# Kernel optimization log

Measured on AMD Instinct MI355X. Metric: run time of the kernel, lower is better.

The kernel has to match this reference:

```python
import jax, jax.numpy as jnp
import numpy as np

H = 24        # attn.heads (Flux)
ENC = 512     # encoder (text) token count, hard-coded in the source via emb[:512]
EPS = 1e-6    # RMSNorm eps


def _rms(x, w):
    # RMSNorm over head_dim (Flux norm_q / norm_k)
    return x * jax.lax.rsqrt(jnp.mean(x * x, axis=-1, keepdims=True) + EPS) * w


def _rope(x, cos, sin):
    # diffusers apply_rotary_emb, use_real=True, unbind_dim=-1
    xr = x.reshape(x.shape[:-1] + (-1, 2))
    rot = jnp.stack([-xr[..., 1], xr[..., 0]], axis=-1).reshape(x.shape)
    return x * cos + rot * sin


def setup_inputs() -> dict:
    key = jax.random.key(0)
    ks = jax.random.split(key, 26)
    B, F, D = 2, 1024, 3072
    hd = D // H
    S = ENC + F
    lin = lambda k: 0.02 * jax.random.normal(k, (D, D), jnp.float32)
    bias = lambda k: 0.02 * jax.random.normal(k, (D,), jnp.float32)
    nw = lambda k: 1.0 + 0.02 * jax.random.normal(k, (hd,), jnp.float32)
    return {
        'hidden_states': jax.random.normal(ks[0], (B, F, D), jnp.float32),
        'encoder_hidden_states': jax.random.normal(ks[1], (B, ENC, D), jnp.float32),
        'rot_cos': jax.random.uniform(ks[2], (S, hd), jnp.float32, minval=-1.0, maxval=1.0),
        'rot_sin': jax.random.uniform(ks[3], (S, hd), jnp.float32, minval=-1.0, maxval=1.0),
        'wq': lin(ks[4]), 'bq': bias(ks[5]),
        'wk': lin(ks[6]), 'bk': bias(ks[7]),
        'wv': lin(ks[8]), 'bv': bias(ks[9]),
        'waq': lin(ks[10]), 'baq': bias(ks[11]),
        'wak': lin(ks[12]), 'bak': bias(ks[13]),
        'wav': lin(ks[14]), 'bav': bias(ks[15]),
        'wo': lin(ks[16]), 'bo': bias(ks[17]),
        'wao': lin(ks[18]), 'bao': bias(ks[19]),
        'nq': nw(ks[20]), 'nk': nw(ks[21]),
        'naq': nw(ks[22]), 'nak': nw(ks[23]),
    }


def reference(hidden_states, encoder_hidden_states, rot_cos, rot_sin,
              wq, bq, wk, bk, wv, bv, waq, baq, wak, bak, wav, bav,
              wo, bo, wao, bao, nq, nk, naq, nak):
    B, F, D = hidden_states.shape
    hd = D // H

    def proj(x, w, b):
        y = x @ w.T + b
        return y.reshape(x.shape[0], -1, H, hd).transpose(0, 2, 1, 3)  # [B,H,S,hd]

    q = _rms(proj(hidden_states, wq, bq), nq)   # [B,H,F,hd]
    k = _rms(proj(hidden_states, wk, bk), nk)
    v = proj(hidden_states, wv, bv)

    # cross-batch mixing: 'b h f d -> 1 h (b f) d' then repeat over batch
    k = jnp.broadcast_to(k.transpose(1, 0, 2, 3).reshape(1, H, B * F, hd), (B, H, B * F, hd))
    v = jnp.broadcast_to(v.transpose(1, 0, 2, 3).reshape(1, H, B * F, hd), (B, H, B * F, hd))

    # key rotary: encoder part once, image part repeated num_components times
    cos_k = jnp.concatenate([rot_cos[:ENC]] + [rot_cos[ENC:]] * B, axis=0)
    sin_k = jnp.concatenate([rot_sin[:ENC]] + [rot_sin[ENC:]] * B, axis=0)

    eq = _rms(proj(encoder_hidden_states, waq, baq), naq)  # [B,H,ENC,hd]
    ek = _rms(proj(encoder_hidden_states, wak, bak), nak)
    ev = proj(encoder_hidden_states, wav, bav)

    q = jnp.concatenate([eq, q], axis=2)  # [B,H,ENC+F,hd]
    k = jnp.concatenate([ek, k], axis=2)  # [B,H,ENC+B*F,hd]
    v = jnp.concatenate([ev, v], axis=2)

    q = _rope(q, rot_cos, rot_sin)
    k = _rope(k, cos_k, sin_k)

    scale = hd ** -0.5
    attn = jax.nn.softmax(jnp.einsum('bhqd,bhkd->bhqk', q, k) * scale, axis=-1)
    out = jnp.einsum('bhqk,bhkd->bhqd', attn, v)
    out = out.transpose(0, 2, 1, 3).reshape(B, -1, D)  # [B,ENC+F,D]

    enc_out = out[:, :ENC] @ wao.T + bao
    hs_out = out[:, ENC:] @ wo.T + bo
    return (hs_out, enc_out)
```

## Files before the change

kernel.cpp:

```cpp
#include <hip/hip_runtime.h>

typedef __attribute__((ext_vector_type(8))) short bf16x8;
typedef __attribute__((ext_vector_type(8))) unsigned short u16x8;
typedef __attribute__((ext_vector_type(4))) unsigned short u16x4;
typedef __attribute__((ext_vector_type(4))) float f32x4;
typedef __attribute__((ext_vector_type(2))) unsigned uint2v;

#define DEV static __device__ __forceinline__

DEV unsigned short f2bf(float f){
  unsigned u = __float_as_uint(f);
  u += 0x7fff + ((u>>16)&1);
  return (unsigned short)(u>>16);
}
DEV float bf2f(unsigned short b){ return __uint_as_float(((unsigned)b)<<16); }
DEV unsigned cvtpk(float lo, float hi){
  unsigned r;
  asm("v_cvt_pk_bf16_f32 %0, %1, %2" : "=v"(r) : "v"(lo), "v"(hi));
  return r;
}

DEV void gll16(const void* g, void* l){
  __builtin_amdgcn_global_load_lds((__attribute__((address_space(1))) unsigned*)(void*)g,
                                   (__attribute__((address_space(3))) unsigned*)l, 16, 0, 0);
}

__global__ void k_cast(const float* __restrict__ x, unsigned short* __restrict__ y, int n4){
  int i = blockIdx.x*256 + threadIdx.x;
  if (i >= n4) return;
  f32x4 v = ((const f32x4*)x)[i];
  u16x4 o = { f2bf(v.x), f2bf(v.y), f2bf(v.z), f2bf(v.w) };
  ((u16x4*)y)[i] = o;
}

__global__ void k_castX2(const float* __restrict__ s0, const float* __restrict__ s1,
                         unsigned short* __restrict__ y){
  unsigned i = blockIdx.x*256 + threadIdx.x;
  const float* s = (i < 1572864u) ? s0 : s1;
  unsigned off = (i < 1572864u) ? i : i - 1572864u;
  f32x4 v = ((const f32x4*)s)[off];
  u16x4 o = { f2bf(v.x), f2bf(v.y), f2bf(v.z), f2bf(v.w) };
  ((u16x4*)y)[i] = o;
}

__global__ void k_castAll(const float* __restrict__ s0, const float* __restrict__ s1,
                          const float* __restrict__ s2, const float* __restrict__ s3,
                          const float* __restrict__ s4, const float* __restrict__ s5,
                          const float* __restrict__ s6, const float* __restrict__ s7,
                          const float* __restrict__ xh, const float* __restrict__ xe,
                          unsigned short* __restrict__ Wb, unsigned short* __restrict__ Xc){
  unsigned i = blockIdx.x*256 + threadIdx.x;
  const float* s; unsigned off; unsigned short* dst; unsigned di;
  if (i < 18874368u){
    unsigned seg = i / 2359296u;
    off = i - seg*2359296u;
    s = seg==0?s0: seg==1?s1: seg==2?s2: seg==3?s3:
        seg==4?s4: seg==5?s5: seg==6?s6: s7;
    dst = Wb; di = i;
  } else {
    unsigned j = i - 18874368u;
    s = (j < 1572864u) ? xh : xe;
    off = (j < 1572864u) ? j : j - 1572864u;
    dst = Xc; di = j;
  }
  f32x4 v = ((const f32x4*)s)[off];
  u16x4 o = { f2bf(v.x), f2bf(v.y), f2bf(v.z), f2bf(v.w) };
  ((u16x4*)dst)[di] = o;
}

__global__ void k_castW2(const float* __restrict__ s0, const float* __restrict__ s1,
                         unsigned short* __restrict__ y){
  unsigned i = blockIdx.x*256 + threadIdx.x;
  unsigned seg = i / 2359296u;
  unsigned off = i - seg*2359296u;
  const float* s = seg==0?s0:s1;
  f32x4 v = ((const f32x4*)s)[off];
  u16x4 o = { f2bf(v.x), f2bf(v.y), f2bf(v.z), f2bf(v.w) };
  ((u16x4*)y)[i] = o;
}

__global__ __launch_bounds__(256) void k_gemmP(
    const unsigned short* __restrict__ X,
    const unsigned short* __restrict__ Wimg, const unsigned short* __restrict__ Wenc,
    const float* __restrict__ b0, const float* __restrict__ b1, const float* __restrict__ b2,
    const float* __restrict__ b3, const float* __restrict__ b4, const float* __restrict__ b5,
    const float* __restrict__ nq_, const float* __restrict__ nk_,
    const float* __restrict__ naq_, const float* __restrict__ nak_,
    const float* __restrict__ cs, const float* __restrict__ sn,
    unsigned short* __restrict__ Qd,
    unsigned short* __restrict__ Kdi, unsigned short* __restrict__ Kde,
    unsigned short* __restrict__ Vdi, unsigned short* __restrict__ Vde,
    int rows_img)
{
  const int K = 3072;
  __shared__ unsigned short SH[16384];
  unsigned short (*As)[4096] = (unsigned short(*)[4096])SH;
  unsigned short (*Bs)[4096] = (unsigned short(*)[4096])(SH + 8192);
  const int t = threadIdx.x, w = t>>6, l = t&63;
  const int li = l&15, g = l>>4;
  const int by = blockIdx.y, bx = blockIdx.x;
  const int sec = by>=48 ? 2 : (by>=24 ? 1 : 0);
  const int hd = by - sec*24;
  const int Cl = hd*128;
  const int R = bx*128;
  const bool img = (R < rows_img);
  const unsigned short* Wp = (img ? Wimg : Wenc) + (long)sec*9437184 + (long)Cl*K;
  const float* bias = img ? ((sec==0)?b0:(sec==1)?b1:b2)
                          : ((sec==0)?b3:(sec==1)?b4:b5);
  const int wr = w>>1, wc = w&1;
  f32x4 acc[4][4] = {};

  auto stage = [&](int buf, int kt){
    const int k0 = kt*32;
    #pragma unroll
    for (int c=0;c<2;c++){
      int row = c*64 + (t>>2);
      int scol = ((t&3)<<3) ^ ((row&3)<<3) ^ (((row>>3)&1)<<4);
      gll16(X + (long)(R+row)*K + k0 + scol, &As[buf][c*2048 + w*512]);
      gll16(Wp + (long)row*K + k0 + scol, &Bs[buf][c*2048 + w*512]);
    }
  };

  stage(0,0);
  int buf = 0;
  for (int kt=0; kt<96; kt++){
    __syncthreads();
    if (kt+1 < 96) stage(buf^1, kt+1);
    bf16x8 a[4], b[4];
    #pragma unroll
    for (int m=0;m<4;m++){
      int ar = wr*64 + m*16 + li;
      int ac = (g<<3) ^ ((ar&3)<<3) ^ (((ar>>3)&1)<<4);
      a[m] = *(const bf16x8*)&As[buf][ar*32 + ac];
      int br = wc*64 + m*16 + li;
      int bc2 = (g<<3) ^ ((br&3)<<3) ^ (((br>>3)&1)<<4);
      b[m] = *(const bf16x8*)&Bs[buf][br*32 + bc2];
    }
    #pragma unroll
    for (int m=0;m<4;m++)
      #pragma unroll
      for (int n=0;n<4;n++)
        acc[m][n] = __builtin_amdgcn_mfma_f32_16x16x32_bf16(a[m], b[n], acc[m][n], 0,0,0);
    buf ^= 1;
  }

  float bias_n[4];
  #pragma unroll
  for (int n=0;n<4;n++) bias_n[n] = bias[Cl + wc*64 + n*16 + li];

  if (sec == 2){
    unsigned short* SHT = SH;
    unsigned short* Vd = img ? Vdi : Vde;
    #pragma unroll
    for (int pass=0; pass<2; pass++){
      __syncthreads();
      if (wc == pass){
        #pragma unroll
        for (int m=0;m<4;m++){
          int tok_l = wr*64 + m*16 + (g<<2);
          #pragma unroll
          for (int n=0;n<4;n++){
            int col_loc = n*16 + li;
            u16x4 v4 = { f2bf(acc[m][n][0]+bias_n[n]), f2bf(acc[m][n][1]+bias_n[n]),
                         f2bf(acc[m][n][2]+bias_n[n]), f2bf(acc[m][n][3]+bias_n[n]) };
            *(u16x4*)&SHT[col_loc*136 + tok_l] = v4;
          }
        }
      }
      __syncthreads();
      int d_loc = t>>2, qtr = t&3;
      int d = pass*64 + d_loc;
      int tok0 = R + qtr*32;
      long base;
      if (img) base = ((long)hd*128 + d)*2048 + tok0;
      else { int t2 = tok0 - rows_img; int b_ = t2>>9, s_ = t2&511;
             base = ((long)(b_*24+hd)*128 + d)*512 + s_; }
      #pragma unroll
      for (int k2=0;k2<4;k2++)
        *(u16x8*)(Vd + base + k2*8) = *(const u16x8*)&SHT[d_loc*136 + qtr*32 + k2*8];
    }
    return;
  }

  float part[4][4];
  #pragma unroll
  for (int m=0;m<4;m++)
    #pragma unroll
    for (int r=0;r<4;r++){
      float s_ = 0.f;
      #pragma unroll
      for (int n=0;n<4;n++){ float v = acc[m][n][r] + bias_n[n]; s_ += v*v; }
      part[m][r] = s_;
    }
  #pragma unroll
  for (int m=0;m<4;m++)
    #pragma unroll
    for (int r=0;r<4;r++){
      part[m][r] += __shfl_xor(part[m][r], 1);
      part[m][r] += __shfl_xor(part[m][r], 2);
      part[m][r] += __shfl_xor(part[m][r], 4);
      part[m][r] += __shfl_xor(part[m][r], 8);
    }
  __syncthreads();
  float* rs = (float*)SH;
  if (li == 0){
    #pragma unroll
    for (int m=0;m<4;m++)
      #pragma unroll
      for (int r=0;r<4;r++)
        rs[(wc*2+wr)*64 + m*16 + g*4 + r] = part[m][r];
  }
  __syncthreads();
  float fac[4][4];
  #pragma unroll
  for (int m=0;m<4;m++)
    #pragma unroll
    for (int r=0;r<4;r++){
      int idx = m*16 + g*4 + r;
      float tot = rs[(0*2+wr)*64 + idx] + rs[(1*2+wr)*64 + idx];
      fac[m][r] = rsqrtf(tot*(1.0f/128.0f) + 1e-6f);
    }

  const float* nw = (sec==0) ? (img ? nq_ : naq_) : (img ? nk_ : nak_);
  const float qs = (sec==0) ? (float)(0.08838834764831845 * 1.4426950408889634) : 1.0f;
  float nw_n[4];
  #pragma unroll
  for (int n=0;n<4;n++) nw_n[n] = nw[wc*64 + n*16 + li];

  unsigned short* Kd = img ? Kdi : Kde;

  #pragma unroll
  for (int m=0;m<4;m++){
    #pragma unroll
    for (int r=0;r<4;r++){
      int row_l = wr*64 + m*16 + g*4 + r;
      int t_row = R + row_l;
      int b_, s_, p_;
      if (img){ b_ = t_row>>10; s_ = t_row&1023; p_ = 512+s_; }
      else { int t2 = t_row - rows_img; b_ = t2>>9; s_ = t2&511; p_ = s_; }
      long didx;
      if (sec==0) didx = (long)(b_*24+hd)*1536 + (img ? 512+s_ : s_);
      else        didx = img ? ((long)hd*2048 + t_row) : ((long)(b_*24+hd)*512 + s_);
      const float* crow = cs + (long)p_*128;
      const float* srow = sn + (long)p_*128;
      unsigned short* drow = ((sec==0)?Qd:Kd) + didx*128;
      #pragma unroll
      for (int n=0;n<4;n++){
        int cl = wc*64 + n*16 + li;
        float x = (acc[m][n][r] + bias_n[n]) * fac[m][r] * nw_n[n];
        float xo = __shfl_xor(x, 1);
        float o_ = x*crow[cl] + ((l&1) ? xo*srow[cl] : -xo*srow[cl]);
        drow[cl] = f2bf(o_*qs);
      }
    }
  }
}

__global__ __launch_bounds__(256) void k_gemmO(
    const unsigned short* __restrict__ X, const unsigned short* __restrict__ Wf,
    float* __restrict__ out, const float* __restrict__ bo, const float* __restrict__ bao)
{
  const int K = 3072;
  __shared__ unsigned short As[2][4096];
  __shared__ unsigned short Bs[2][4096];
  const int t = threadIdx.x, w = t>>6, l = t&63;
  unsigned wid = blockIdx.x + 24u*blockIdx.y;
  unsigned xc = wid & 7, ii = wid >> 3;
  unsigned xg = xc & 1, yg = xc >> 1;
  int bx = (int)(xg*12 + ii%12);
  int by = (int)(yg*6 + ii/12);
  const bool enc = bx >= 16;
  const unsigned short* Wp = Wf + (enc ? 9437184 : 0);
  const float* bias = enc ? bao : bo;
  const int R = bx*128, C = by*128;
  long xbase, obase;
  if (!enc){ xbase = (long)(R>>10)*1536 + 512 + (R&1023); obase = (long)R*3072; }
  else { int Rp = R-2048; xbase = (long)(Rp>>9)*1536 + (Rp&511); obase = 6291456 + (long)Rp*3072; }
  const int wr = w>>1, wc = w&1;
  f32x4 acc[4][4] = {};

  auto stage = [&](int buf, int kt){
    const int k0 = kt*32;
    #pragma unroll
    for (int c=0;c<2;c++){
      int row = c*64 + (t>>2);
      int scol = ((t&3)<<3) ^ ((row&3)<<3) ^ (((row>>3)&1)<<4);
      gll16(X + (xbase+row)*K + k0 + scol, &As[buf][c*2048 + w*512]);
      gll16(Wp + (long)(C+row)*K + k0 + scol, &Bs[buf][c*2048 + w*512]);
    }
  };

  stage(0,0);
  int buf = 0;
  for (int kt=0; kt<96; kt++){
    __syncthreads();
    if (kt+1 < 96) stage(buf^1, kt+1);
    bf16x8 a[4], b[4];
    #pragma unroll
    for (int m=0;m<4;m++){
      int ar = wr*64 + m*16 + (l&15);
      int ac = ((l>>4)<<3) ^ ((ar&3)<<3) ^ (((ar>>3)&1)<<4);
      a[m] = *(const bf16x8*)&As[buf][ar*32 + ac];
      int br = wc*64 + m*16 + (l&15);
      int bc2 = ((l>>4)<<3) ^ ((br&3)<<3) ^ (((br>>3)&1)<<4);
      b[m] = *(const bf16x8*)&Bs[buf][br*32 + bc2];
    }
    #pragma unroll
    for (int m=0;m<4;m++)
      #pragma unroll
      for (int n=0;n<4;n++)
        acc[m][n] = __builtin_amdgcn_mfma_f32_16x16x32_bf16(a[m], b[n], acc[m][n], 0,0,0);
    buf ^= 1;
  }

  #pragma unroll
  for (int m=0;m<4;m++){
    int rl = wr*64 + m*16 + ((l>>4)<<2);
    #pragma unroll
    for (int n=0;n<4;n++){
      int col = C + wc*64 + n*16 + (l&15);
      float bvv = bias[col];
      #pragma unroll
      for (int r=0;r<4;r++)
        out[obase + (long)(rl+r)*3072 + col] = acc[m][n][r] + bvv;
    }
  }
}

__global__ __launch_bounds__(256) void k_attn(
    const unsigned short* __restrict__ Q,
    const unsigned short* __restrict__ Ke, const unsigned short* __restrict__ Ki,
    const unsigned short* __restrict__ Ve, const unsigned short* __restrict__ Vi,
    unsigned short* __restrict__ AO)
{
  __shared__ unsigned short Ks[8192];
  __shared__ unsigned short Vs[8192];
  __shared__ unsigned short Ps[4][1408];
  const int t = threadIdx.x, w = t>>6, l = t&63;
  unsigned wid = blockIdx.x + 24u*blockIdx.y + 576u*blockIdx.z;
  unsigned xc = wid & 7, ii = wid >> 3;
  int h = (int)(xc*3 + ii/48);
  unsigned rem = ii % 48;
  int b = (int)(rem/24);
  int qx = (int)(rem%24);
  const int bh = b*24 + h;
  const int q0 = qx*64 + w*16;
  const int g = l>>4;

  auto stageK = [&](int jt){
    const unsigned short* ksrc = (jt < 8) ? Ke + ((long)bh*512 + jt*64)*128
                                          : Ki + ((long)h*2048 + (jt-8)*64)*128;
    #pragma unroll
    for (int c=0;c<4;c++){
      int row = c*16 + (t>>4);
      int col = ((t&15)<<3) ^ ((row&7)<<3);
      gll16(ksrc + row*128 + col, &Ks[c*2048 + w*512]);
    }
  };
  auto stageV = [&](int jt){
    const unsigned short* vsrc; long vstr;
    if (jt < 8){ vsrc = Ve + (long)bh*65536 + jt*64; vstr = 512; }
    else { vsrc = Vi + (long)h*262144 + (jt-8)*64; vstr = 2048; }
    #pragma unroll
    for (int c=0;c<4;c++){
      int row = c*32 + (t>>3);
      int col = ((t&7)<<3) ^ ((row&7)<<3);
      gll16(vsrc + (long)row*vstr + col, &Vs[c*2048 + w*512]);
    }
  };

  bf16x8 qf[4];
  {
    const unsigned short* qp = Q + ((long)bh*1536 + q0 + (l&15))*128 + (g<<3);
    #pragma unroll
    for (int kc=0;kc<4;kc++) qf[kc] = *(const bf16x8*)(qp + kc*32);
  }
  f32x4 o[8] = {};
  float mx = -1e30f;
  float ls = 0.f;

  stageK(0);
  for (int jt=0; jt<40; jt++){
    __syncthreads();
    stageV(jt);

    f32x4 sf[4];
    __builtin_amdgcn_s_setprio(1);
    #pragma unroll
    for (int ct=0;ct<4;ct++){
      f32x4 s = {};
      #pragma unroll
      for (int kc=0;kc<4;kc++){
        int krow = ct*16 + (l&15);
        int kcol = (kc*32 + (g<<3)) ^ ((krow&7)<<3);
        bf16x8 kb = *(const bf16x8*)&Ks[krow*128 + kcol];
        s = __builtin_amdgcn_mfma_f32_16x16x32_bf16(kb, qf[kc], s, 0,0,0);
      }
      sf[ct] = s;
    }
    __builtin_amdgcn_s_setprio(0);

    float pm = sf[0][0];
    #pragma unroll
    for (int ct=0;ct<4;ct++)
      #pragma unroll
      for (int r=0;r<4;r++) pm = fmaxf(pm, sf[ct][r]);
    if (!__all(pm <= mx + 8.0f)){
      float tmax = pm;
      tmax = fmaxf(tmax, __shfl_xor(tmax, 16));
      tmax = fmaxf(tmax, __shfl_xor(tmax, 32));
      float mn = fmaxf(mx, tmax);
      float al = exp2f(mx - mn);
      mx = mn;
      ls *= al;
      #pragma unroll
      for (int r=0;r<4;r++){
        float alo = __shfl(al, (l&48) | ((g<<2)+r));
        #pragma unroll
        for (int f=0;f<8;f++) o[f][r] *= alo;
      }
    }
    #pragma unroll
    for (int ct=0;ct<4;ct++){
      float p0 = exp2f(sf[ct][0]-mx), p1 = exp2f(sf[ct][1]-mx);
      float p2 = exp2f(sf[ct][2]-mx), p3 = exp2f(sf[ct][3]-mx);
      ls += (p0+p1)+(p2+p3);
      uint2v pk = { cvtpk(p0,p1), cvtpk(p2,p3) };
      *(uint2v*)&Ps[w][(l&15)*88 + ct*16 + (g<<2)] = pk;
    }
    __syncthreads();

    if (jt+1 < 40) stageK(jt+1);

    bf16x8 pa[2];
    #pragma unroll
    for (int kc=0;kc<2;kc++)
      pa[kc] = *(const bf16x8*)&Ps[w][(l&15)*88 + kc*32 + (g<<3)];
    __builtin_amdgcn_s_setprio(1);
    #pragma unroll
    for (int f=0;f<8;f++){
      #pragma unroll
      for (int kc=0;kc<2;kc++){
        int vrow = f*16 + (l&15);
        int vcol = (kc*32 + (g<<3)) ^ ((vrow&7)<<3);
        bf16x8 vb = *(const bf16x8*)&Vs[vrow*64 + vcol];
        o[f] = __builtin_amdgcn_mfma_f32_16x16x32_bf16(pa[kc], vb, o[f], 0,0,0);
      }
    }
    __builtin_amdgcn_s_setprio(0);
  }

  ls += __shfl_xor(ls, 16);
  ls += __shfl_xor(ls, 32);
  #pragma unroll
  for (int r=0;r<4;r++){
    float lso = __shfl(ls, (l&48) | ((g<<2)+r));
    float inv = 1.0f/lso;
    int qrow = q0 + (g<<2) + r;
    #pragma unroll
    for (int f=0;f<8;f++){
      AO[((long)b*1536 + qrow)*3072 + h*128 + f*16 + (l&15)] = f2bf(o[f][r]*inv);
    }
  }
}

extern "C" void kernel_launch(void* const* d_in, const int* in_sizes, int n_in,
                              void* d_out, int out_size, void* d_ws, size_t ws_size,
                              hipStream_t stream)
{
  const float* hs  = (const float*)d_in[0];
  const float* ehs = (const float*)d_in[1];
  const float* rc  = (const float*)d_in[2];
  const float* rs_ = (const float*)d_in[3];
  const float* wq = (const float*)d_in[4];  const float* bq = (const float*)d_in[5];
  const float* wk = (const float*)d_in[6];  const float* bk = (const float*)d_in[7];
  const float* wv = (const float*)d_in[8];  const float* bv = (const float*)d_in[9];
  const float* waq= (const float*)d_in[10]; const float* baq= (const float*)d_in[11];
  const float* wak= (const float*)d_in[12]; const float* bak= (const float*)d_in[13];
  const float* wav= (const float*)d_in[14]; const float* bav= (const float*)d_in[15];
  const float* wo = (const float*)d_in[16]; const float* bo = (const float*)d_in[17];
  const float* wao= (const float*)d_in[18]; const float* bao= (const float*)d_in[19];
  const float* nq = (const float*)d_in[20]; const float* nk = (const float*)d_in[21];
  const float* naq= (const float*)d_in[22]; const float* nak= (const float*)d_in[23];

  char* p = (char*)d_ws;
  auto alloc = [&](size_t bytes){ char* r = p; p += bytes; return r; };

  if (ws_size >= (size_t)226492416){
    unsigned short* Xh = (unsigned short*)alloc(12582912);
    unsigned short* Xe = (unsigned short*)alloc(6291456);
    unsigned short* Wb = (unsigned short*)alloc(150994944);
    unsigned short* Qb = (unsigned short*)alloc(18874368);
    unsigned short* Ke = (unsigned short*)alloc(6291456);
    unsigned short* Ki = (unsigned short*)alloc(12582912);
    unsigned short* Ve = (unsigned short*)alloc(6291456);
    unsigned short* Vi = (unsigned short*)alloc(12582912);
    unsigned short* AO = Xh;
    (void)Xe;

    k_castAll<<<82944,256,0,stream>>>(wq, wk, wv, waq, wak, wav, wo, wao, hs, ehs, Wb, Xh);

    k_gemmP<<<dim3(24,72),256,0,stream>>>(Xh, Wb, Wb + (long)3*9437184,
                                          bq, bk, bv, baq, bak, bav,
                                          nq, nk, naq, nak, rc, rs_,
                                          Qb, Ki, Ke, Vi, Ve, 2048);

    k_attn<<<dim3(24,24,2),256,0,stream>>>(Qb, Ke, Ki, Ve, Vi, AO);

    k_gemmO<<<dim3(24,24),256,0,stream>>>(AO, Wb + (long)6*9437184, (float*)d_out, bo, bao);
  } else {
    unsigned short* Xh = (unsigned short*)alloc(12582912);
    unsigned short* Xe = (unsigned short*)alloc(6291456);
    unsigned short* Wb = (unsigned short*)alloc(56623104);
    unsigned short* Qb = (unsigned short*)alloc(18874368);
    unsigned short* Ke = (unsigned short*)alloc(6291456);
    unsigned short* Ki = (unsigned short*)alloc(12582912);
    unsigned short* Ve = (unsigned short*)alloc(6291456);
    unsigned short* Vi = (unsigned short*)alloc(12582912);
    unsigned short* AO = Xh;

    k_castX2<<<9216,256,0,stream>>>(hs, ehs, Xh);

    k_cast<<<9216,256,0,stream>>>(wq, Wb, 2359296);
    k_cast<<<9216,256,0,stream>>>(wk, Wb + 9437184, 2359296);
    k_cast<<<9216,256,0,stream>>>(wv, Wb + 18874368, 2359296);
    k_gemmP<<<dim3(16,72),256,0,stream>>>(Xh, Wb, Wb,
                                          bq, bk, bv, bq, bk, bv,
                                          nq, nk, nq, nk, rc, rs_,
                                          Qb, Ki, Ke, Vi, Ve, 1<<28);

    k_cast<<<9216,256,0,stream>>>(waq, Wb, 2359296);
    k_cast<<<9216,256,0,stream>>>(wak, Wb + 9437184, 2359296);
    k_cast<<<9216,256,0,stream>>>(wav, Wb + 18874368, 2359296);
    k_gemmP<<<dim3(8,72),256,0,stream>>>(Xe, Wb, Wb,
                                         baq, bak, bav, baq, bak, bav,
                                         naq, nak, naq, nak, rc, rs_,
                                         Qb, Ki, Ke, Vi, Ve, 0);

    k_attn<<<dim3(24,24,2),256,0,stream>>>(Qb, Ke, Ki, Ve, Vi, AO);

    k_castW2<<<18432,256,0,stream>>>(wo, wao, Wb);
    k_gemmO<<<dim3(24,24),256,0,stream>>>(AO, Wb, (float*)d_out, bo, bao);
  }
}
```

Before: 654.9 us.

## Split QKV projection into 256x256-tile GEMM plus separate norm/rope/transposition passes

Replaces the fused projection GEMM (which applied RMSNorm, RoPE and layout writes in its epilogue) with a larger 256x256 tile, 512-thread GEMM that writes a plain bf16 Y buffer. Separate small kernels then apply RMSNorm+RoPE to Q/K, folding softmax scale times log2e into Q, and transpose V into the attention layout. The output-projection weight cast is moved to after attention so it reuses the weight buffer. This adds extra passes over the projection output and more launches in exchange for better tile reuse in the dominant GEMM, and it needs a larger workspace, otherwise the fallback path runs.

```diff
diff --git a/kernel.cpp b/kernel.cpp
--- a/kernel.cpp
+++ b/kernel.cpp
@@ -43,22 +43,20 @@
   ((u16x4*)y)[i] = o;
 }
 
-__global__ void k_castAll(const float* __restrict__ s0, const float* __restrict__ s1,
+__global__ void k_castA6X(const float* __restrict__ s0, const float* __restrict__ s1,
                           const float* __restrict__ s2, const float* __restrict__ s3,
                           const float* __restrict__ s4, const float* __restrict__ s5,
-                          const float* __restrict__ s6, const float* __restrict__ s7,
                           const float* __restrict__ xh, const float* __restrict__ xe,
                           unsigned short* __restrict__ Wb, unsigned short* __restrict__ Xc){
   unsigned i = blockIdx.x*256 + threadIdx.x;
   const float* s; unsigned off; unsigned short* dst; unsigned di;
-  if (i < 18874368u){
+  if (i < 14155776u){
     unsigned seg = i / 2359296u;
     off = i - seg*2359296u;
-    s = seg==0?s0: seg==1?s1: seg==2?s2: seg==3?s3:
-        seg==4?s4: seg==5?s5: seg==6?s6: s7;
+    s = seg==0?s0: seg==1?s1: seg==2?s2: seg==3?s3: seg==4?s4: s5;
     dst = Wb; di = i;
   } else {
-    unsigned j = i - 18874368u;
+    unsigned j = i - 14155776u;
     s = (j < 1572864u) ? xh : xe;
     off = (j < 1572864u) ? j : j - 1572864u;
     dst = Xc; di = j;
@@ -77,6 +75,160 @@
   f32x4 v = ((const f32x4*)s)[off];
   u16x4 o = { f2bf(v.x), f2bf(v.y), f2bf(v.z), f2bf(v.w) };
   ((u16x4*)y)[i] = o;
+}
+
+__global__ __launch_bounds__(512) void k_gemmP256(
+    const unsigned short* __restrict__ X,
+    const unsigned short* __restrict__ Wimg, const unsigned short* __restrict__ Wenc,
+    const float* __restrict__ b0, const float* __restrict__ b1, const float* __restrict__ b2,
+    const float* __restrict__ b3, const float* __restrict__ b4, const float* __restrict__ b5,
+    unsigned short* __restrict__ Y, int rows_img)
+{
+  __shared__ unsigned short LDS[2][32768];
+  const int t = threadIdx.x, w = t>>6, l = t&63;
+  const int li = l&15, g = l>>4;
+  const int wr = w>>2, wc = w&3;
+  const int bxr = blockIdx.x, by = blockIdx.y;
+  const int R = bxr*256;
+  const int sec = by/12;
+  const int Cn = (by%12)*256;
+  const bool img = (R < rows_img);
+  const unsigned short* Wbase = (img ? Wimg : Wenc) + (long)sec*9437184 + (long)Cn*3072;
+  const float* bias = img ? ((sec==0)?b0:(sec==1)?b1:b2)
+                          : ((sec==0)?b3:(sec==1)?b4:b5);
+
+  f32x4 acc[8][4] = {};
+
+  auto stageC = [&](int buf, int kt, int c){
+    int row = (c&3)*64 + (t>>3);
+    int sgrp = (t&7) ^ (row&7);
+    const unsigned short* src = (c<4)
+        ? X + (long)(R+row)*3072 + kt*64 + sgrp*8
+        : Wbase + (long)row*3072 + kt*64 + sgrp*8;
+    gll16(src, &LDS[buf][(c<4?0:16384) + (c&3)*4096 + t*8]);
+  };
+
+  #pragma unroll
+  for (int c=0;c<8;c++) stageC(0, 0, c);
+
+  for (int kt=0; kt<48; kt++){
+    __syncthreads();
+    const int buf = kt&1;
+    const unsigned short* Ab = &LDS[buf][0];
+    const unsigned short* Bb = &LDS[buf][16384];
+
+    bf16x8 Bf[4][2];
+    #pragma unroll
+    for (int fc=0;fc<4;fc++)
+      #pragma unroll
+      for (int kh=0;kh<2;kh++){
+        int brow = wc*64 + fc*16 + li;
+        int bgrp = ((kh<<2) + g) ^ (brow&7);
+        Bf[fc][kh] = *(const bf16x8*)&Bb[brow*64 + bgrp*8];
+      }
+    if (kt+1 < 48){
+      #pragma unroll
+      for (int c=0;c<4;c++) stageC(buf^1, kt+1, c);
+    }
+
+    #pragma unroll
+    for (int p=0;p<4;p++){
+      bf16x8 Af[2][2];
+      #pragma unroll
+      for (int f2=0;f2<2;f2++)
+        #pragma unroll
+        for (int kh=0;kh<2;kh++){
+          int arow = wr*128 + (2*p+f2)*16 + li;
+          int agrp = ((kh<<2) + g) ^ (arow&7);
+          Af[f2][kh] = *(const bf16x8*)&Ab[arow*64 + agrp*8];
+        }
+      if (p==0 && kt+1 < 48){
+        #pragma unroll
+        for (int c=4;c<8;c++) stageC(buf^1, kt+1, c);
+      }
+      __builtin_amdgcn_s_setprio(1);
+      #pragma unroll
+      for (int f2=0;f2<2;f2++)
+        #pragma unroll
+        for (int fc=0;fc<4;fc++)
+          #pragma unroll
+          for (int kh=0;kh<2;kh++)
+            acc[2*p+f2][fc] = __builtin_amdgcn_mfma_f32_16x16x32_bf16(
+                                Af[f2][kh], Bf[fc][kh], acc[2*p+f2][fc], 0,0,0);
+      __builtin_amdgcn_s_setprio(0);
+    }
+  }
+
+  float bias_n[4];
+  #pragma unroll
+  for (int fc=0;fc<4;fc++) bias_n[fc] = bias[Cn + wc*64 + fc*16 + li];
+  #pragma unroll
+  for (int fr=0;fr<8;fr++){
+    int row = R + wr*128 + fr*16 + g*4;
+    #pragma unroll
+    for (int fc=0;fc<4;fc++){
+      long col = (long)by*256 + wc*64 + fc*16 + li;
+      #pragma unroll
+      for (int r=0;r<4;r++)
+        Y[(long)(row+r)*9216 + col] = f2bf(acc[fr][fc][r] + bias_n[fc]);
+    }
+  }
+}
+
+__global__ void k_ppqk(const unsigned short* __restrict__ Y, int ystr, int yoff,
+    const float* __restrict__ nw,
+    const float* __restrict__ cs, const float* __restrict__ sn, unsigned short* __restrict__ dst,
+    int T_log2, int tpb_log2, int dest_off, int S, int no_batch,
+    int pos_off, int pos_mask, float qscale)
+{
+  int rid = blockIdx.x*4 + (threadIdx.x>>6);
+  int l = threadIdx.x & 63;
+  int h = rid >> T_log2, tk = rid & ((1<<T_log2)-1);
+  unsigned pair = *(const unsigned*)(Y + (long)tk*ystr + yoff + h*128 + 2*l);
+  float x0 = bf2f((unsigned short)(pair&0xffff));
+  float x1 = bf2f((unsigned short)(pair>>16));
+  float ss = x0*x0 + x1*x1;
+  #pragma unroll
+  for (int m=1;m<64;m<<=1) ss += __shfl_xor(ss, m);
+  float rr = rsqrtf(ss*(1.0f/128.0f) + 1e-6f);
+  x0 *= rr*nw[2*l]; x1 *= rr*nw[2*l+1];
+  int p = pos_off + (tk & pos_mask);
+  float c0 = cs[p*128 + 2*l], c1 = cs[p*128 + 2*l+1];
+  float s0 = sn[p*128 + 2*l], s1 = sn[p*128 + 2*l+1];
+  float o0 = (x0*c0 - x1*s0)*qscale;
+  float o1 = (x1*c1 + x0*s1)*qscale;
+  long idx;
+  if (no_batch) idx = (long)h*S + tk;
+  else {
+    int b = tk >> tpb_log2;
+    int sq = dest_off + (tk & ((1<<tpb_log2)-1));
+    idx = (long)(b*24+h)*S + sq;
+  }
+  unsigned out = (unsigned)f2bf(o0) | ((unsigned)f2bf(o1)<<16);
+  *(unsigned*)(dst + idx*128 + 2*l) = out;
+}
+
+__global__ void k_ppv(const unsigned short* __restrict__ Y, int ystr, int yoff,
+                      unsigned short* __restrict__ Vt, int vstr, int no_batch)
+{
+  __shared__ unsigned short tileS[64][136];
+  int t = threadIdx.x, h = blockIdx.y;
+  int tile0 = blockIdx.x*64;
+  #pragma unroll
+  for (int c=0;c<4;c++){
+    int j = c*16 + (t>>4), col = (t&15)*8;
+    *(u16x8*)&tileS[j][col] = *(const u16x8*)(Y + (long)(tile0+j)*ystr + yoff + h*128 + col);
+  }
+  __syncthreads();
+  int d = t>>1, half = t&1;
+  unsigned short tmp[32];
+  #pragma unroll
+  for (int i=0;i<32;i++) tmp[i] = tileS[half*32+i][d];
+  long base;
+  if (no_batch) base = ((long)h*128 + d)*vstr + tile0 + half*32;
+  else { int b = tile0>>9; base = ((long)(b*24+h)*128 + d)*vstr + (tile0&511) + half*32; }
+  #pragma unroll
+  for (int k=0;k<4;k++) *(u16x8*)(Vt + base + k*8) = *(const u16x8*)&tmp[k*8];
 }
 
 __global__ __launch_bounds__(256) void k_gemmP(
@@ -483,31 +635,41 @@
   const float* nq = (const float*)d_in[20]; const float* nk = (const float*)d_in[21];
   const float* naq= (const float*)d_in[22]; const float* nak= (const float*)d_in[23];
 
+  const float qsc = (float)(0.08838834764831845 * 1.4426950408889634);
+
   char* p = (char*)d_ws;
   auto alloc = [&](size_t bytes){ char* r = p; p += bytes; return r; };
 
-  if (ws_size >= (size_t)226492416){
+  if (ws_size >= (size_t)245366784){
     unsigned short* Xh = (unsigned short*)alloc(12582912);
     unsigned short* Xe = (unsigned short*)alloc(6291456);
-    unsigned short* Wb = (unsigned short*)alloc(150994944);
+    unsigned short* Wb = (unsigned short*)alloc(113246208);
+    unsigned short* Yb = (unsigned short*)alloc(56623104);
     unsigned short* Qb = (unsigned short*)alloc(18874368);
     unsigned short* Ke = (unsigned short*)alloc(6291456);
     unsigned short* Ki = (unsigned short*)alloc(12582912);
     unsigned short* Ve = (unsigned short*)alloc(6291456);
     unsigned short* Vi = (unsigned short*)alloc(12582912);
     unsigned short* AO = Xh;
+    unsigned short* Ye = Yb + (long)2048*9216;
     (void)Xe;
 
-    k_castAll<<<82944,256,0,stream>>>(wq, wk, wv, waq, wak, wav, wo, wao, hs, ehs, Wb, Xh);
-
-    k_gemmP<<<dim3(24,72),256,0,stream>>>(Xh, Wb, Wb + (long)3*9437184,
-                                          bq, bk, bv, baq, bak, bav,
-                                          nq, nk, naq, nak, rc, rs_,
-                                          Qb, Ki, Ke, Vi, Ve, 2048);
+    k_castA6X<<<64512,256,0,stream>>>(wq, wk, wv, waq, wak, wav, hs, ehs, Wb, Xh);
+
+    k_gemmP256<<<dim3(12,36),512,0,stream>>>(Xh, Wb, Wb + (long)3*9437184,
+                                             bq, bk, bv, baq, bak, bav, Yb, 2048);
+
+    k_ppqk<<<12288,256,0,stream>>>(Yb, 9216, 0,    nq,  rc, rs_, Qb, 11, 10, 512, 1536, 0, 512, 1023, qsc);
+    k_ppqk<<<12288,256,0,stream>>>(Yb, 9216, 3072, nk,  rc, rs_, Ki, 11, 0,  0,   2048, 1, 512, 1023, 1.0f);
+    k_ppv<<<dim3(32,24),256,0,stream>>>(Yb, 9216, 6144, Vi, 2048, 1);
+    k_ppqk<<<6144,256,0,stream>>>(Ye, 9216, 0,    naq, rc, rs_, Qb, 10, 9, 0, 1536, 0, 0, 511, qsc);
+    k_ppqk<<<6144,256,0,stream>>>(Ye, 9216, 3072, nak, rc, rs_, Ke, 10, 9, 0, 512,  0, 0, 511, 1.0f);
+    k_ppv<<<dim3(16,24),256,0,stream>>>(Ye, 9216, 6144, Ve, 512, 0);
 
     k_attn<<<dim3(24,24,2),256,0,stream>>>(Qb, Ke, Ki, Ve, Vi, AO);
 
-    k_gemmO<<<dim3(24,24),256,0,stream>>>(AO, Wb + (long)6*9437184, (float*)d_out, bo, bao);
+    k_castW2<<<18432,256,0,stream>>>(wo, wao, Wb);
+    k_gemmO<<<dim3(24,24),256,0,stream>>>(AO, Wb, (float*)d_out, bo, bao);
   } else {
     unsigned short* Xh = (unsigned short*)alloc(12582912);
     unsigned short* Xe = (unsigned short*)alloc(6291456);
```

Result: faster. 586.0 us, median of 2 (-10.5%).
